# Optimization experiments

Measured on AMD Instinct MI355X. Metric: run time of the kernel, lower is better.

## Reference

```python
import jax, jax.numpy as jnp
import numpy as np

MAX_POINTS = 32
EPS = 1e-5


def setup_inputs() -> dict:
    key = jax.random.key(0)
    k1, k2, k3, k4, k5, k6 = jax.random.split(key, 6)
    M, P, C_IN, C_OUT = 40000, MAX_POINTS, 4, 64
    voxel_features = jax.random.normal(k1, (M, P, C_IN), dtype=jnp.float32)
    voxel_num_points = jax.random.randint(k2, (M,), 0, MAX_POINTS, dtype=jnp.int32)
    # Linear(C_in, C_out) params (PyTorch default init scale ~ U(-1/sqrt(fan_in), ...))
    lim = 1.0 / np.sqrt(C_IN)
    W = jax.random.uniform(k3, (C_OUT, C_IN), minval=-lim, maxval=lim, dtype=jnp.float32)
    b = jax.random.uniform(k4, (C_OUT,), minval=-lim, maxval=lim, dtype=jnp.float32)
    # BatchNorm1d affine params
    gamma = jnp.ones((C_OUT,), dtype=jnp.float32)
    beta = jnp.zeros((C_OUT,), dtype=jnp.float32)
    return {"voxel_features": voxel_features, "voxel_num_points": voxel_num_points,
            "W": W, "b": b, "gamma": gamma, "beta": beta}


def _vfe(x, n, W, b, gamma, beta):
    # x: (M, P, C_in), n: (M,) valid point counts
    mask = (jnp.arange(MAX_POINTS)[None, :] < n[:, None])            # (M, P)
    maskf = mask.astype(x.dtype)[..., None]                          # (M, P, 1)
    h = jnp.einsum('mpc,oc->mpo', x, W) + b                          # (M, P, C_out)
    h = h * maskf                                                    # zero invalid slots
    # BatchNorm1d (training-mode batch stats) over valid points only
    n_valid = jnp.maximum(jnp.sum(maskf), 1.0)
    mu = jnp.sum(h, axis=(0, 1)) / n_valid                           # (C_out,)
    d = (h - mu) * maskf
    var = jnp.sum(d * d, axis=(0, 1)) / n_valid                      # biased var, as BN
    hn = d * jax.lax.rsqrt(var + EPS) * gamma + beta * maskf
    hn = jax.nn.relu(hn) * maskf
    # per-voxel mean over valid points; voxels with n==0 output zeros
    counts = jnp.maximum(n.astype(x.dtype), 1.0)[:, None]
    return jnp.sum(hn, axis=1) / counts                              # (M, C_out)


def reference(voxel_features, voxel_num_points, W, b, gamma, beta):
    return _vfe(voxel_features, voxel_num_points, W, b, gamma, beta)
```

## Files before the change

### kernel.cpp

```cpp
#include <hip/hip_runtime.h>

#define MAX_POINTS 32
#define C_OUT 64
#define EPS 1e-5f

#define NMOM 15
#define NSET 16
#define WS_FLOATS (NSET * 16)
#define STATS_BLOCKS 512

__global__ __launch_bounds__(256) void vfe_stats(
    const float* __restrict__ x, const int* __restrict__ vnp,
    float* __restrict__ ws, int M)
{
    const int tid    = blockIdx.x * 256 + threadIdx.x;
    const int stride = gridDim.x * 256;
    const int total  = M * MAX_POINTS;

    float a[NMOM];
    #pragma unroll
    for (int i = 0; i < NMOM; ++i) a[i] = 0.f;

    const float4* __restrict__ xq = (const float4*)x;
    for (int i = tid; i < total; i += stride) {
        const float4 q0 = xq[i];
        const int   n   = vnp[i >> 5];
        const float mk  = ((i & 31) < n) ? 1.f : 0.f;
        const float qx = q0.x * mk, qy = q0.y * mk, qz = q0.z * mk, qw = q0.w * mk;
        a[0] += qx; a[1] += qy; a[2] += qz; a[3] += qw;
        a[4]  = fmaf(qx, qx, a[4]);
        a[5]  = fmaf(qx, qy, a[5]);
        a[6]  = fmaf(qx, qz, a[6]);
        a[7]  = fmaf(qx, qw, a[7]);
        a[8]  = fmaf(qy, qy, a[8]);
        a[9]  = fmaf(qy, qz, a[9]);
        a[10] = fmaf(qy, qw, a[10]);
        a[11] = fmaf(qz, qz, a[11]);
        a[12] = fmaf(qz, qw, a[12]);
        a[13] = fmaf(qw, qw, a[13]);
        a[14] += mk;
    }

    #pragma unroll
    for (int i = 0; i < NMOM; ++i) {
        float v = a[i];
        #pragma unroll
        for (int off = 32; off > 0; off >>= 1)
            v += __shfl_down(v, off, 64);
        a[i] = v;
    }

    __shared__ float bl[4][NMOM];
    const int lane = threadIdx.x & 63;
    const int wid  = threadIdx.x >> 6;
    if (lane == 0) {
        #pragma unroll
        for (int i = 0; i < NMOM; ++i) bl[wid][i] = a[i];
    }
    __syncthreads();
    if (threadIdx.x < NMOM) {
        const int i = threadIdx.x;
        const int set = blockIdx.x & (NSET - 1);
        atomicAdd(&ws[set * 16 + i], bl[0][i] + bl[1][i] + bl[2][i] + bl[3][i]);
    }
}

template<int NP>
__device__ __forceinline__ float voxel_body(
    const float4* __restrict__ xq, int n, float4 wA, float c0)
{
    float acc0 = 0.f, acc1 = 0.f, acc2 = 0.f, acc3 = 0.f;
    #pragma unroll
    for (int p = 0; p < NP; ++p) {
        const float4 q = xq[p];
        float v = fmaf(q.x, wA.x, fmaf(q.y, wA.y,
                  fmaf(q.z, wA.z, fmaf(q.w, wA.w, c0))));
        v = fmaxf(v, 0.f);
        if (p >= NP - 8) v = (p < n) ? v : 0.f;
        if      ((p & 3) == 0) acc0 += v;
        else if ((p & 3) == 1) acc1 += v;
        else if ((p & 3) == 2) acc2 += v;
        else                   acc3 += v;
    }
    return (acc0 + acc1) + (acc2 + acc3);
}

__global__ __launch_bounds__(256) void vfe_out(
    const float* __restrict__ x, const int* __restrict__ vnp,
    const float* __restrict__ W, const float* __restrict__ b,
    const float* __restrict__ gamma, const float* __restrict__ beta,
    const float* __restrict__ ws, float* __restrict__ out, int M)
{
    const int lane = threadIdx.x & 63;
    const int wid  = threadIdx.x >> 6;
    const int gw   = blockIdx.x * 4 + wid;

    const float4* __restrict__ ws4 = (const float4*)ws;
    float4 m4[4];
    #pragma unroll
    for (int k = 0; k < 4; ++k) {
        float4 s = ws4[k];
        #pragma unroll
        for (int j = 1; j < NSET; ++j) {
            const float4 t = ws4[j * 4 + k];
            s.x += t.x; s.y += t.y; s.z += t.z; s.w += t.w;
        }
        m4[k] = s;
    }
    const float mom[NMOM] = { m4[0].x, m4[0].y, m4[0].z, m4[0].w,
                              m4[1].x, m4[1].y, m4[1].z, m4[1].w,
                              m4[2].x, m4[2].y, m4[2].z, m4[2].w,
                              m4[3].x, m4[3].y, m4[3].z };

    const float4 w4  = ((const float4*)W)[lane];
    const float bias = b[lane];
    const float cnt  = mom[14];
    const float nv   = fmaxf(cnt, 1.0f);
    const float wdots = w4.x*mom[0] + w4.y*mom[1] + w4.z*mom[2] + w4.w*mom[3];
    const float mu   = (wdots + cnt * bias) / nv;
    const float q2 = mom[4]*w4.x*w4.x + mom[8]*w4.y*w4.y + mom[11]*w4.z*w4.z + mom[13]*w4.w*w4.w
                   + 2.f*(mom[5]*w4.x*w4.y + mom[6]*w4.x*w4.z + mom[7]*w4.x*w4.w
                        + mom[9]*w4.y*w4.z + mom[10]*w4.y*w4.w + mom[12]*w4.z*w4.w);
    const float SS  = q2 + 2.f*bias*wdots + cnt*bias*bias;
    const float var = fmaxf(SS / nv - mu * mu, 0.f);
    const float A   = gamma[lane] * rsqrtf(var + EPS);
    const float B   = fmaf(-mu, A, beta[lane]);
    const float4 wA = make_float4(w4.x * A, w4.y * A, w4.z * A, w4.w * A);
    const float  c0 = fmaf(bias, A, B);

    const int m_base = gw * 4;
    if (m_base >= M) return;

    int4 n4;
    if (m_base + 3 < M) {
        n4 = *(const int4*)(vnp + m_base);
    } else {
        n4.x = vnp[m_base];
        n4.y = (m_base + 1 < M) ? vnp[m_base + 1] : 0;
        n4.z = (m_base + 2 < M) ? vnp[m_base + 2] : 0;
        n4.w = (m_base + 3 < M) ? vnp[m_base + 3] : 0;
    }
    const int ns[4] = { n4.x, n4.y, n4.z, n4.w };

    #pragma unroll
    for (int v = 0; v < 4; ++v) {
        const int m = m_base + v;
        if (m >= M) break;
        const int n = ns[v];
        const float4* __restrict__ xq = (const float4*)x + (size_t)m * MAX_POINTS;
        float acc;
        if      (n > 24) acc = voxel_body<32>(xq, n, wA, c0);
        else if (n > 16) acc = voxel_body<24>(xq, n, wA, c0);
        else if (n >  8) acc = voxel_body<16>(xq, n, wA, c0);
        else if (n >  0) acc = voxel_body< 8>(xq, n, wA, c0);
        else             acc = 0.f;
        const float rn = 1.0f / fmaxf((float)n, 1.0f);
        out[(size_t)m * C_OUT + lane] = acc * rn;
    }
}

extern "C" void kernel_launch(void* const* d_in, const int* in_sizes, int n_in,
                              void* d_out, int out_size, void* d_ws, size_t ws_size,
                              hipStream_t stream) {
    const float* x     = (const float*)d_in[0];
    const int*   vnp   = (const int*)  d_in[1];
    const float* W     = (const float*)d_in[2];
    const float* b     = (const float*)d_in[3];
    const float* gamma = (const float*)d_in[4];
    const float* beta  = (const float*)d_in[5];
    float* out = (float*)d_out;
    float* ws  = (float*)d_ws;
    const int M = in_sizes[1];

    hipMemsetAsync(d_ws, 0, WS_FLOATS * sizeof(float), stream);
    vfe_stats<<<STATS_BLOCKS, 256, 0, stream>>>(x, vnp, ws, M);
    const int nwaves = (M + 3) / 4;
    const int nblk   = (nwaves + 3) / 4;
    vfe_out<<<nblk, 256, 0, stream>>>(x, vnp, W, b, gamma, beta, ws, out, M);
}
```

Measured before the change: 115.5 us.

## Unroll stats loop, double stats grid, and process eight voxels per wave

Doubles the stats grid and unrolls its grid-stride loop by two so each thread keeps more loads in flight. In the output kernel the moment reduction now runs once per block through shared memory instead of in every thread, and each wave handles eight voxels instead of four. This amortizes the per-wave BN setup cost. The trade-off is half as many output blocks, which lowers parallelism, plus an added __syncthreads. An empty if-block is left behind.

Result: no change. 113.4 us (-1.8%).

```diff
diff --git a/kernel.cpp b/kernel.cpp
--- a/kernel.cpp
+++ b/kernel.cpp
@@ -7,7 +7,7 @@
 #define NMOM 15
 #define NSET 16
 #define WS_FLOATS (NSET * 16)
-#define STATS_BLOCKS 512
+#define STATS_BLOCKS 1024
 
 __global__ __launch_bounds__(256) void vfe_stats(
     const float* __restrict__ x, const int* __restrict__ vnp,
@@ -22,11 +22,36 @@
     for (int i = 0; i < NMOM; ++i) a[i] = 0.f;
 
     const float4* __restrict__ xq = (const float4*)x;
-    for (int i = tid; i < total; i += stride) {
+
+    int i = tid;
+    for (; i + stride < total; i += 2 * stride) {
+        const int i2 = i + stride;
         const float4 q0 = xq[i];
-        const int   n   = vnp[i >> 5];
-        const float mk  = ((i & 31) < n) ? 1.f : 0.f;
-        const float qx = q0.x * mk, qy = q0.y * mk, qz = q0.z * mk, qw = q0.w * mk;
+        const float4 q1 = xq[i2];
+        const int    n0 = vnp[i  >> 5];
+        const int    n1 = vnp[i2 >> 5];
+        const float mk0 = ((i  & 31) < n0) ? 1.f : 0.f;
+        const float mk1 = ((i2 & 31) < n1) ? 1.f : 0.f;
+        const float ax = q0.x*mk0, ay = q0.y*mk0, az = q0.z*mk0, aw = q0.w*mk0;
+        const float bx = q1.x*mk1, by = q1.y*mk1, bz = q1.z*mk1, bw = q1.w*mk1;
+        a[0] += ax + bx; a[1] += ay + by; a[2] += az + bz; a[3] += aw + bw;
+        a[4]  = fmaf(ax, ax, fmaf(bx, bx, a[4]));
+        a[5]  = fmaf(ax, ay, fmaf(bx, by, a[5]));
+        a[6]  = fmaf(ax, az, fmaf(bx, bz, a[6]));
+        a[7]  = fmaf(ax, aw, fmaf(bx, bw, a[7]));
+        a[8]  = fmaf(ay, ay, fmaf(by, by, a[8]));
+        a[9]  = fmaf(ay, az, fmaf(by, bz, a[9]));
+        a[10] = fmaf(ay, aw, fmaf(by, bw, a[10]));
+        a[11] = fmaf(az, az, fmaf(bz, bz, a[11]));
+        a[12] = fmaf(az, aw, fmaf(bz, bw, a[12]));
+        a[13] = fmaf(aw, aw, fmaf(bw, bw, a[13]));
+        a[14] += mk0 + mk1;
+    }
+    for (; i < total; i += stride) {
+        const float4 q0 = xq[i];
+        const int    n  = vnp[i >> 5];
+        const float  mk = ((i & 31) < n) ? 1.f : 0.f;
+        const float qx = q0.x*mk, qy = q0.y*mk, qz = q0.z*mk, qw = q0.w*mk;
         a[0] += qx; a[1] += qy; a[2] += qz; a[3] += qw;
         a[4]  = fmaf(qx, qx, a[4]);
         a[5]  = fmaf(qx, qy, a[5]);
@@ -42,12 +67,12 @@
     }
 
     #pragma unroll
-    for (int i = 0; i < NMOM; ++i) {
-        float v = a[i];
+    for (int k = 0; k < NMOM; ++k) {
+        float v = a[k];
         #pragma unroll
         for (int off = 32; off > 0; off >>= 1)
             v += __shfl_down(v, off, 64);
-        a[i] = v;
+        a[k] = v;
     }
 
     __shared__ float bl[4][NMOM];
@@ -55,13 +80,13 @@
     const int wid  = threadIdx.x >> 6;
     if (lane == 0) {
         #pragma unroll
-        for (int i = 0; i < NMOM; ++i) bl[wid][i] = a[i];
+        for (int k = 0; k < NMOM; ++k) bl[wid][k] = a[k];
     }
     __syncthreads();
     if (threadIdx.x < NMOM) {
-        const int i = threadIdx.x;
+        const int k = threadIdx.x;
         const int set = blockIdx.x & (NSET - 1);
-        atomicAdd(&ws[set * 16 + i], bl[0][i] + bl[1][i] + bl[2][i] + bl[3][i]);
+        atomicAdd(&ws[set * 16 + k], bl[0][k] + bl[1][k] + bl[2][k] + bl[3][k]);
     }
 }
 
@@ -93,24 +118,21 @@
 {
     const int lane = threadIdx.x & 63;
     const int wid  = threadIdx.x >> 6;
-    const int gw   = blockIdx.x * 4 + wid;
-
-    const float4* __restrict__ ws4 = (const float4*)ws;
-    float4 m4[4];
-    #pragma unroll
-    for (int k = 0; k < 4; ++k) {
-        float4 s = ws4[k];
-        #pragma unroll
-        for (int j = 1; j < NSET; ++j) {
-            const float4 t = ws4[j * 4 + k];
-            s.x += t.x; s.y += t.y; s.z += t.z; s.w += t.w;
-        }
-        m4[k] = s;
-    }
-    const float mom[NMOM] = { m4[0].x, m4[0].y, m4[0].z, m4[0].w,
-                              m4[1].x, m4[1].y, m4[1].z, m4[1].w,
-                              m4[2].x, m4[2].y, m4[2].z, m4[2].w,
-                              m4[3].x, m4[3].y, m4[3].z };
+
+    __shared__ float smom[NMOM];
+    if (threadIdx.x < NSET) {
+    }
+    if (threadIdx.x < NMOM) {
+        const int k = threadIdx.x;
+        float s = 0.f;
+        #pragma unroll
+        for (int j = 0; j < NSET; ++j) s += ws[j * 16 + k];
+        smom[k] = s;
+    }
+    __syncthreads();
+    float mom[NMOM];
+    #pragma unroll
+    for (int k = 0; k < NMOM; ++k) mom[k] = smom[k];
 
     const float4 w4  = ((const float4*)W)[lane];
     const float bias = b[lane];
@@ -128,22 +150,24 @@
     const float4 wA = make_float4(w4.x * A, w4.y * A, w4.z * A, w4.w * A);
     const float  c0 = fmaf(bias, A, B);
 
-    const int m_base = gw * 4;
+    const int gw     = blockIdx.x * 4 + wid;
+    const int m_base = gw * 8;
     if (m_base >= M) return;
 
-    int4 n4;
-    if (m_base + 3 < M) {
-        n4 = *(const int4*)(vnp + m_base);
+    int ns[8];
+    if (m_base + 7 < M) {
+        const int4 na = *(const int4*)(vnp + m_base);
+        const int4 nb = *(const int4*)(vnp + m_base + 4);
+        ns[0]=na.x; ns[1]=na.y; ns[2]=na.z; ns[3]=na.w;
+        ns[4]=nb.x; ns[5]=nb.y; ns[6]=nb.z; ns[7]=nb.w;
     } else {
-        n4.x = vnp[m_base];
-        n4.y = (m_base + 1 < M) ? vnp[m_base + 1] : 0;
-        n4.z = (m_base + 2 < M) ? vnp[m_base + 2] : 0;
-        n4.w = (m_base + 3 < M) ? vnp[m_base + 3] : 0;
-    }
-    const int ns[4] = { n4.x, n4.y, n4.z, n4.w };
-
-    #pragma unroll
-    for (int v = 0; v < 4; ++v) {
+        #pragma unroll
+        for (int v = 0; v < 8; ++v)
+            ns[v] = (m_base + v < M) ? vnp[m_base + v] : 0;
+    }
+
+    #pragma unroll
+    for (int v = 0; v < 8; ++v) {
         const int m = m_base + v;
         if (m >= M) break;
         const int n = ns[v];
@@ -174,7 +198,7 @@
 
     hipMemsetAsync(d_ws, 0, WS_FLOATS * sizeof(float), stream);
     vfe_stats<<<STATS_BLOCKS, 256, 0, stream>>>(x, vnp, ws, M);
-    const int nwaves = (M + 3) / 4;
+    const int nwaves = (M + 7) / 8;
     const int nblk   = (nwaves + 3) / 4;
     vfe_out<<<nblk, 256, 0, stream>>>(x, vnp, W, b, gamma, beta, ws, out, M);
 }
```
